# Performance work log

Measured on AMD Instinct MI355X. Metric: run time of the kernel, lower is better.

Reference implementation:

```python
import jax, jax.numpy as jnp
import numpy as np

NODE_SIZE = 500000
LINK_SIZE = 500
DIM = 128
NORM_P = 1
MARGIN = 1.0
BATCH = 16384


def setup_inputs() -> dict:
    key = jax.random.key(0)
    k1, k2, k3, k4, k5, k6, k7, k8 = jax.random.split(key, 8)
    ur_e = 6.0 / np.sqrt(DIM)
    ur_m = 6.0 / DIM
    node_w = jax.random.uniform(k1, (NODE_SIZE, DIM), jnp.float32, -ur_e, ur_e)
    link_w = jax.random.uniform(k2, (LINK_SIZE, DIM), jnp.float32, -ur_e, ur_e)
    transfer_w = jax.random.uniform(k3, (LINK_SIZE, DIM * DIM), jnp.float32, -ur_m, ur_m)
    sp = jax.random.randint(k4, (BATCH,), 0, NODE_SIZE)
    tp = jax.random.randint(k5, (BATCH,), 0, NODE_SIZE)
    sn = jax.random.randint(k6, (BATCH,), 0, NODE_SIZE)
    tn = jax.random.randint(k7, (BATCH,), 0, NODE_SIZE)
    r = jax.random.randint(k8, (BATCH,), 0, LINK_SIZE)
    return {"node_w": node_w, "link_w": link_w, "transfer_w": transfer_w,
            "sp": sp, "tp": tp, "sn": sn, "tn": tn, "r": r}


def _distance(node_w, link_w, transfer_w, s, r, t):
    # gather embeddings
    s_emb = node_w[s]                      # [B, D]
    t_emb = node_w[t]                      # [B, D]
    r_emb = link_w[r]                      # [B, D]
    M = transfer_w[r].reshape(-1, DIM, DIM)  # [B, D, D]
    # per-sample (1xD)x(DxD) matvec: e @ M
    s_proj = jnp.einsum('bd,bde->be', s_emb, M)
    t_proj = jnp.einsum('bd,bde->be', t_emb, M)
    diff = s_proj + r_emb - t_proj
    if NORM_P == 1:
        return jnp.sum(jnp.abs(diff), axis=1)
    return jnp.sum(jnp.abs(diff) ** NORM_P, axis=1) ** (1.0 / NORM_P)


def reference(node_w, link_w, transfer_w, sp, tp, sn, tn, r):
    pos = _distance(node_w, link_w, transfer_w, sp, r, tp)
    neg = _distance(node_w, link_w, transfer_w, sn, r, tn)
    # MarginRankingLoss with target = -1: max(0, (pos - neg) + margin)
    loss = jnp.maximum(pos - neg + MARGIN, 0.0)
    return jnp.mean(loss)
```

## Files before the change

### kernel.cpp

```cpp
#include <hip/hip_runtime.h>

#define BATCH 16384
#define DIM 128
#define NLINK 500
#define EHALF 64
#define NS 16
#define DP_STRIDE 132
#define CAP 128

#define WS_COUNTS 0
#define WS_BUCKET 512
#define WS_P0 (512 + NLINK * CAP)
#define WS_P1 (WS_P0 + BATCH)
#define WS_N0 (WS_P1 + BATCH)
#define WS_N1 (WS_N0 + BATCH)

__global__ void k_zero(int* wsi, float* out) {
    int t = threadIdx.x;
    wsi[WS_COUNTS + t] = 0;
    if (t == 0) out[0] = 0.0f;
}

__global__ void k_scatter(const int* __restrict__ r, int* wsi) {
    int i = blockIdx.x * blockDim.x + threadIdx.x;
    if (i < BATCH) {
        int rr = r[i];
        int pos = atomicAdd(&wsi[WS_COUNTS + rr], 1);
        wsi[WS_BUCKET + rr * CAP + pos] = i;
    }
}

__global__ __launch_bounds__(256, 3) void k_main(
    const float* __restrict__ node_w, const float* __restrict__ link_w,
    const float* __restrict__ transfer_w,
    const int* __restrict__ sp, const int* __restrict__ tp,
    const int* __restrict__ sn, const int* __restrict__ tn,
    int* __restrict__ wsi)
{
    __shared__ float Ms[DIM * EHALF];
    __shared__ float dp[NS * DP_STRIDE];
    __shared__ float dn[NS * DP_STRIDE];
    __shared__ float remb[EHALF];

    const int link = blockIdx.x >> 1;
    const int h = blockIdx.x & 1;
    const int t = threadIdx.x;

    {
        const float4* G = (const float4*)transfer_w;
        float4* Ms4 = (float4*)Ms;
        #pragma unroll
        for (int i = 0; i < 8; i++) {
            int c = t + 256 * i;
            Ms4[c] = G[link * 4096 + (c >> 4) * 32 + h * 16 + (c & 15)];
        }
    }
    if (t < 16)
        ((float4*)remb)[t] = ((const float4*)(link_w + link * DIM + h * EHALF))[t];

    const int count = wsi[WS_COUNTS + link];
    const int base  = WS_BUCKET + link * CAP;
    const int g = t >> 4;
    const int q = t & 15;
    float* dpr = dp + g * DP_STRIDE;
    float* dnr = dn + g * DP_STRIDE;
    float* pOut = (float*)(wsi + (h ? WS_P1 : WS_P0));
    float* nOut = (float*)(wsi + (h ? WS_N1 : WS_N0));

    __syncthreads();

    for (int k = 0; k < count; k += NS) {
        const int myk = k + g;
        const bool active = (myk < count);
        int b = 0;
        if (active) {
            b = wsi[base + myk];
            const float4* a  = (const float4*)(node_w + (size_t)sp[b] * DIM);
            const float4* c2 = (const float4*)(node_w + (size_t)tp[b] * DIM);
            float4 a0 = a[q], a1 = a[q + 16], c0 = c2[q], c1 = c2[q + 16];
            float4 w0, w1;
            w0.x = a0.x - c0.x; w0.y = a0.y - c0.y; w0.z = a0.z - c0.z; w0.w = a0.w - c0.w;
            w1.x = a1.x - c1.x; w1.y = a1.y - c1.y; w1.z = a1.z - c1.z; w1.w = a1.w - c1.w;
            ((float4*)dpr)[q] = w0;
            ((float4*)dpr)[q + 16] = w1;
            const float4* e2 = (const float4*)(node_w + (size_t)sn[b] * DIM);
            const float4* f2 = (const float4*)(node_w + (size_t)tn[b] * DIM);
            float4 e0 = e2[q], e1 = e2[q + 16], f0 = f2[q], f1 = f2[q + 16];
            w0.x = e0.x - f0.x; w0.y = e0.y - f0.y; w0.z = e0.z - f0.z; w0.w = e0.w - f0.w;
            w1.x = e1.x - f1.x; w1.y = e1.y - f1.y; w1.z = e1.z - f1.z; w1.w = e1.w - f1.w;
            ((float4*)dnr)[q] = w0;
            ((float4*)dnr)[q + 16] = w1;
        }
        __syncthreads();

        float4 accp = {0.f, 0.f, 0.f, 0.f};
        float4 accn = {0.f, 0.f, 0.f, 0.f};
        const float4* M4 = (const float4*)Ms;
        #pragma unroll 4
        for (int d4 = 0; d4 < 32; d4++) {
            float4 vp = ((const float4*)dpr)[d4];
            float4 vn = ((const float4*)dnr)[d4];
            float4 m0 = M4[(4 * d4 + 0) * 16 + q];
            float4 m1 = M4[(4 * d4 + 1) * 16 + q];
            float4 m2 = M4[(4 * d4 + 2) * 16 + q];
            float4 m3 = M4[(4 * d4 + 3) * 16 + q];
            accp.x = fmaf(m0.x, vp.x, accp.x); accp.y = fmaf(m0.y, vp.x, accp.y);
            accp.z = fmaf(m0.z, vp.x, accp.z); accp.w = fmaf(m0.w, vp.x, accp.w);
            accn.x = fmaf(m0.x, vn.x, accn.x); accn.y = fmaf(m0.y, vn.x, accn.y);
            accn.z = fmaf(m0.z, vn.x, accn.z); accn.w = fmaf(m0.w, vn.x, accn.w);
            accp.x = fmaf(m1.x, vp.y, accp.x); accp.y = fmaf(m1.y, vp.y, accp.y);
            accp.z = fmaf(m1.z, vp.y, accp.z); accp.w = fmaf(m1.w, vp.y, accp.w);
            accn.x = fmaf(m1.x, vn.y, accn.x); accn.y = fmaf(m1.y, vn.y, accn.y);
            accn.z = fmaf(m1.z, vn.y, accn.z); accn.w = fmaf(m1.w, vn.y, accn.w);
            accp.x = fmaf(m2.x, vp.z, accp.x); accp.y = fmaf(m2.y, vp.z, accp.y);
            accp.z = fmaf(m2.z, vp.z, accp.z); accp.w = fmaf(m2.w, vp.z, accp.w);
            accn.x = fmaf(m2.x, vn.z, accn.x); accn.y = fmaf(m2.y, vn.z, accn.y);
            accn.z = fmaf(m2.z, vn.z, accn.z); accn.w = fmaf(m2.w, vn.z, accn.w);
            accp.x = fmaf(m3.x, vp.w, accp.x); accp.y = fmaf(m3.y, vp.w, accp.y);
            accp.z = fmaf(m3.z, vp.w, accp.z); accp.w = fmaf(m3.w, vp.w, accp.w);
            accn.x = fmaf(m3.x, vn.w, accn.x); accn.y = fmaf(m3.y, vn.w, accn.y);
            accn.z = fmaf(m3.z, vn.w, accn.z); accn.w = fmaf(m3.w, vn.w, accn.w);
        }

        float4 re = ((const float4*)remb)[q];
        float lp = fabsf(accp.x + re.x) + fabsf(accp.y + re.y) +
                   fabsf(accp.z + re.z) + fabsf(accp.w + re.w);
        float ln = fabsf(accn.x + re.x) + fabsf(accn.y + re.y) +
                   fabsf(accn.z + re.z) + fabsf(accn.w + re.w);
        #pragma unroll
        for (int o = 8; o >= 1; o >>= 1) {
            lp += __shfl_xor(lp, o, 16);
            ln += __shfl_xor(ln, o, 16);
        }
        if (active && q == 0) {
            pOut[b] = lp;
            nOut[b] = ln;
        }
        __syncthreads();
    }
}

__global__ void k_final(const int* __restrict__ wsi, float* __restrict__ out) {
    const float* p0 = (const float*)(wsi + WS_P0);
    const float* p1 = (const float*)(wsi + WS_P1);
    const float* n0 = (const float*)(wsi + WS_N0);
    const float* n1 = (const float*)(wsi + WS_N1);
    int i = blockIdx.x * 256 + threadIdx.x;
    float l = 0.0f;
    if (i < BATCH) {
        float pos = p0[i] + p1[i];
        float neg = n0[i] + n1[i];
        l = fmaxf(pos - neg + 1.0f, 0.0f);
    }
    #pragma unroll
    for (int o = 32; o >= 1; o >>= 1) l += __shfl_xor(l, o, 64);
    __shared__ float w[4];
    if ((threadIdx.x & 63) == 0) w[threadIdx.x >> 6] = l;
    __syncthreads();
    if (threadIdx.x == 0)
        atomicAdd(out, (w[0] + w[1] + w[2] + w[3]) * (1.0f / BATCH));
}

extern "C" void kernel_launch(void* const* d_in, const int* in_sizes, int n_in,
                              void* d_out, int out_size, void* d_ws, size_t ws_size,
                              hipStream_t stream) {
    const float* node_w     = (const float*)d_in[0];
    const float* link_w     = (const float*)d_in[1];
    const float* transfer_w = (const float*)d_in[2];
    const int* sp = (const int*)d_in[3];
    const int* tp = (const int*)d_in[4];
    const int* sn = (const int*)d_in[5];
    const int* tn = (const int*)d_in[6];
    const int* r  = (const int*)d_in[7];
    float* out = (float*)d_out;
    int* wsi = (int*)d_ws;

    k_zero<<<1, 512, 0, stream>>>(wsi, out);
    k_scatter<<<(BATCH + 255) / 256, 256, 0, stream>>>(r, wsi);
    k_main<<<NLINK * 2, 256, 0, stream>>>(node_w, link_w, transfer_w,
                                          sp, tp, sn, tn, wsi);
    k_final<<<(BATCH + 255) / 256, 256, 0, stream>>>(wsi, out);
}
```

Before: 349.5 us.

## Fuse bucketing, projection and loss into one per-link kernel with full-matrix LDS

Replaces the zero, scatter, main and final kernels with a single kernel that runs one 512-thread block per link. Each block scans the whole relation index array and builds its own sample list in LDS, so there is no global scatter pass or workspace. The full 128x128 transfer matrix is staged into LDS with async global-to-LDS loads, so each node embedding row is gathered once instead of once per column half. The margin loss is reduced inside the block and added with one atomic per block, with no intermediate pos/neg buffers. The cost is that every block re-reads the index array, and the larger LDS footprint lowers occupancy.

Measured after the change: 341.7 us. -2.2%, faster.

```diff
diff --git a/kernel.cpp b/kernel.cpp
--- a/kernel.cpp
+++ b/kernel.cpp
@@ -3,107 +3,102 @@
 #define BATCH 16384
 #define DIM 128
 #define NLINK 500
-#define EHALF 64
 #define NS 16
 #define DP_STRIDE 132
 #define CAP 128
 
-#define WS_COUNTS 0
-#define WS_BUCKET 512
-#define WS_P0 (512 + NLINK * CAP)
-#define WS_P1 (WS_P0 + BATCH)
-#define WS_N0 (WS_P1 + BATCH)
-#define WS_N1 (WS_N0 + BATCH)
-
-__global__ void k_zero(int* wsi, float* out) {
-    int t = threadIdx.x;
-    wsi[WS_COUNTS + t] = 0;
-    if (t == 0) out[0] = 0.0f;
+__device__ __forceinline__ void gload_lds16(const float* g, float* l) {
+    __builtin_amdgcn_global_load_lds(
+        (const __attribute__((address_space(1))) void*)g,
+        (__attribute__((address_space(3))) void*)l, 16, 0, 0);
 }
 
-__global__ void k_scatter(const int* __restrict__ r, int* wsi) {
-    int i = blockIdx.x * blockDim.x + threadIdx.x;
-    if (i < BATCH) {
-        int rr = r[i];
-        int pos = atomicAdd(&wsi[WS_COUNTS + rr], 1);
-        wsi[WS_BUCKET + rr * CAP + pos] = i;
-    }
+__global__ void k_init(float* __restrict__ out) {
+    if (threadIdx.x == 0) out[0] = 0.0f;
 }
 
-__global__ __launch_bounds__(256, 3) void k_main(
+__global__ __launch_bounds__(512, 2) void k_fused(
     const float* __restrict__ node_w, const float* __restrict__ link_w,
     const float* __restrict__ transfer_w,
     const int* __restrict__ sp, const int* __restrict__ tp,
     const int* __restrict__ sn, const int* __restrict__ tn,
-    int* __restrict__ wsi)
+    const int* __restrict__ r, float* __restrict__ out)
 {
-    __shared__ float Ms[DIM * EHALF];
+    __shared__ float Ms[DIM * DIM];
     __shared__ float dp[NS * DP_STRIDE];
     __shared__ float dn[NS * DP_STRIDE];
-    __shared__ float remb[EHALF];
+    __shared__ float remb[DIM];
+    __shared__ int   slist[CAP];
+    __shared__ int   cnt;
+    __shared__ float lossbuf[NS];
 
-    const int link = blockIdx.x >> 1;
-    const int h = blockIdx.x & 1;
+    const int link = blockIdx.x;
     const int t = threadIdx.x;
+    const int g = t >> 5;
+    const int q = t & 31;
+
+    if (t == 0) cnt = 0;
+    __syncthreads();
+
+    int4 rv[8];
+    #pragma unroll
+    for (int j = 0; j < 8; j++) rv[j] = ((const int4*)r)[j * 512 + t];
 
     {
-        const float4* G = (const float4*)transfer_w;
-        float4* Ms4 = (float4*)Ms;
+        const float* src = transfer_w + (size_t)link * (DIM * DIM);
         #pragma unroll
         for (int i = 0; i < 8; i++) {
-            int c = t + 256 * i;
-            Ms4[c] = G[link * 4096 + (c >> 4) * 32 + h * 16 + (c & 15)];
+            const int c = (t + 512 * i) * 4;
+            gload_lds16(src + c, Ms + c);
         }
     }
-    if (t < 16)
-        ((float4*)remb)[t] = ((const float4*)(link_w + link * DIM + h * EHALF))[t];
+    float4 rl;
+    if (t < 32) rl = ((const float4*)(link_w + (size_t)link * DIM))[q];
 
-    const int count = wsi[WS_COUNTS + link];
-    const int base  = WS_BUCKET + link * CAP;
-    const int g = t >> 4;
-    const int q = t & 15;
+    #pragma unroll
+    for (int j = 0; j < 8; j++) {
+        const int bi = (j * 512 + t) * 4;
+        if (rv[j].x == link) slist[atomicAdd(&cnt, 1)] = bi;
+        if (rv[j].y == link) slist[atomicAdd(&cnt, 1)] = bi + 1;
+        if (rv[j].z == link) slist[atomicAdd(&cnt, 1)] = bi + 2;
+        if (rv[j].w == link) slist[atomicAdd(&cnt, 1)] = bi + 3;
+    }
+    if (t < 32) ((float4*)remb)[q] = rl;
+    __syncthreads();
+
+    const int count = cnt;
     float* dpr = dp + g * DP_STRIDE;
     float* dnr = dn + g * DP_STRIDE;
-    float* pOut = (float*)(wsi + (h ? WS_P1 : WS_P0));
-    float* nOut = (float*)(wsi + (h ? WS_N1 : WS_N0));
-
-    __syncthreads();
+    const float4* M4 = (const float4*)Ms;
+    float groupSum = 0.0f;
 
     for (int k = 0; k < count; k += NS) {
-        const int myk = k + g;
-        const bool active = (myk < count);
-        int b = 0;
+        const bool active = (k + g < count);
         if (active) {
-            b = wsi[base + myk];
-            const float4* a  = (const float4*)(node_w + (size_t)sp[b] * DIM);
-            const float4* c2 = (const float4*)(node_w + (size_t)tp[b] * DIM);
-            float4 a0 = a[q], a1 = a[q + 16], c0 = c2[q], c1 = c2[q + 16];
-            float4 w0, w1;
-            w0.x = a0.x - c0.x; w0.y = a0.y - c0.y; w0.z = a0.z - c0.z; w0.w = a0.w - c0.w;
-            w1.x = a1.x - c1.x; w1.y = a1.y - c1.y; w1.z = a1.z - c1.z; w1.w = a1.w - c1.w;
-            ((float4*)dpr)[q] = w0;
-            ((float4*)dpr)[q + 16] = w1;
-            const float4* e2 = (const float4*)(node_w + (size_t)sn[b] * DIM);
-            const float4* f2 = (const float4*)(node_w + (size_t)tn[b] * DIM);
-            float4 e0 = e2[q], e1 = e2[q + 16], f0 = f2[q], f1 = f2[q + 16];
-            w0.x = e0.x - f0.x; w0.y = e0.y - f0.y; w0.z = e0.z - f0.z; w0.w = e0.w - f0.w;
-            w1.x = e1.x - f1.x; w1.y = e1.y - f1.y; w1.z = e1.z - f1.z; w1.w = e1.w - f1.w;
-            ((float4*)dnr)[q] = w0;
-            ((float4*)dnr)[q + 16] = w1;
+            const int b = slist[k + g];
+            const float4* A = (const float4*)(node_w + (size_t)sp[b] * DIM);
+            const float4* C = (const float4*)(node_w + (size_t)tp[b] * DIM);
+            float4 a0 = A[q], c0 = C[q];
+            float4 w;
+            w.x = a0.x - c0.x; w.y = a0.y - c0.y; w.z = a0.z - c0.z; w.w = a0.w - c0.w;
+            ((float4*)dpr)[q] = w;
+            const float4* E = (const float4*)(node_w + (size_t)sn[b] * DIM);
+            const float4* F = (const float4*)(node_w + (size_t)tn[b] * DIM);
+            float4 e0 = E[q], f0 = F[q];
+            w.x = e0.x - f0.x; w.y = e0.y - f0.y; w.z = e0.z - f0.z; w.w = e0.w - f0.w;
+            ((float4*)dnr)[q] = w;
         }
-        __syncthreads();
 
         float4 accp = {0.f, 0.f, 0.f, 0.f};
         float4 accn = {0.f, 0.f, 0.f, 0.f};
-        const float4* M4 = (const float4*)Ms;
         #pragma unroll 4
         for (int d4 = 0; d4 < 32; d4++) {
             float4 vp = ((const float4*)dpr)[d4];
             float4 vn = ((const float4*)dnr)[d4];
-            float4 m0 = M4[(4 * d4 + 0) * 16 + q];
-            float4 m1 = M4[(4 * d4 + 1) * 16 + q];
-            float4 m2 = M4[(4 * d4 + 2) * 16 + q];
-            float4 m3 = M4[(4 * d4 + 3) * 16 + q];
+            float4 m0 = M4[(4 * d4 + 0) * 32 + q];
+            float4 m1 = M4[(4 * d4 + 1) * 32 + q];
+            float4 m2 = M4[(4 * d4 + 2) * 32 + q];
+            float4 m3 = M4[(4 * d4 + 3) * 32 + q];
             accp.x = fmaf(m0.x, vp.x, accp.x); accp.y = fmaf(m0.y, vp.x, accp.y);
             accp.z = fmaf(m0.z, vp.x, accp.z); accp.w = fmaf(m0.w, vp.x, accp.w);
             accn.x = fmaf(m0.x, vn.x, accn.x); accn.y = fmaf(m0.y, vn.x, accn.y);
@@ -123,42 +118,23 @@
         }
 
         float4 re = ((const float4*)remb)[q];
-        float lp = fabsf(accp.x + re.x) + fabsf(accp.y + re.y) +
-                   fabsf(accp.z + re.z) + fabsf(accp.w + re.w);
-        float ln = fabsf(accn.x + re.x) + fabsf(accn.y + re.y) +
-                   fabsf(accn.z + re.z) + fabsf(accn.w + re.w);
+        float v = fabsf(accp.x + re.x) + fabsf(accp.y + re.y)
+                + fabsf(accp.z + re.z) + fabsf(accp.w + re.w)
+                - fabsf(accn.x + re.x) - fabsf(accn.y + re.y)
+                - fabsf(accn.z + re.z) - fabsf(accn.w + re.w);
         #pragma unroll
-        for (int o = 8; o >= 1; o >>= 1) {
-            lp += __shfl_xor(lp, o, 16);
-            ln += __shfl_xor(ln, o, 16);
-        }
-        if (active && q == 0) {
-            pOut[b] = lp;
-            nOut[b] = ln;
-        }
-        __syncthreads();
+        for (int o = 16; o >= 1; o >>= 1) v += __shfl_xor(v, o, 32);
+        if (active && q == 0) groupSum += fmaxf(v + 1.0f, 0.0f);
     }
-}
 
-__global__ void k_final(const int* __restrict__ wsi, float* __restrict__ out) {
-    const float* p0 = (const float*)(wsi + WS_P0);
-    const float* p1 = (const float*)(wsi + WS_P1);
-    const float* n0 = (const float*)(wsi + WS_N0);
-    const float* n1 = (const float*)(wsi + WS_N1);
-    int i = blockIdx.x * 256 + threadIdx.x;
-    float l = 0.0f;
-    if (i < BATCH) {
-        float pos = p0[i] + p1[i];
-        float neg = n0[i] + n1[i];
-        l = fmaxf(pos - neg + 1.0f, 0.0f);
+    if (q == 0) lossbuf[g] = groupSum;
+    __syncthreads();
+    if (t == 0) {
+        float s = 0.0f;
+        #pragma unroll
+        for (int i = 0; i < NS; i++) s += lossbuf[i];
+        atomicAdd(out, s * (1.0f / BATCH));
     }
-    #pragma unroll
-    for (int o = 32; o >= 1; o >>= 1) l += __shfl_xor(l, o, 64);
-    __shared__ float w[4];
-    if ((threadIdx.x & 63) == 0) w[threadIdx.x >> 6] = l;
-    __syncthreads();
-    if (threadIdx.x == 0)
-        atomicAdd(out, (w[0] + w[1] + w[2] + w[3]) * (1.0f / BATCH));
 }
 
 extern "C" void kernel_launch(void* const* d_in, const int* in_sizes, int n_in,
@@ -173,11 +149,9 @@
     const int* tn = (const int*)d_in[6];
     const int* r  = (const int*)d_in[7];
     float* out = (float*)d_out;
-    int* wsi = (int*)d_ws;
+    (void)d_ws; (void)ws_size;
 
-    k_zero<<<1, 512, 0, stream>>>(wsi, out);
-    k_scatter<<<(BATCH + 255) / 256, 256, 0, stream>>>(r, wsi);
-    k_main<<<NLINK * 2, 256, 0, stream>>>(node_w, link_w, transfer_w,
-                                          sp, tp, sn, tn, wsi);
-    k_final<<<(BATCH + 255) / 256, 256, 0, stream>>>(wsi, out);
+    k_init<<<1, 64, 0, stream>>>(out);
+    k_fused<<<NLINK, 512, 0, stream>>>(node_w, link_w, transfer_w,
+                                       sp, tp, sn, tn, r, out);
 }
```
